# Performance work log

Hardware: AMD Instinct MI355X
Metric: run time of the kernel (lower is better)

The kernel has to match this reference:

```python
import jax, jax.numpy as jnp
import numpy as np

NQ = 8          # qubits -> 2^8 = 256 amplitudes
B = 32768       # batch

# ---- gate matrices (torchquantum conventions) ----

def _rx(t):
    c = jnp.cos(t / 2).astype(jnp.complex64)
    s = jnp.sin(t / 2).astype(jnp.complex64)
    return jnp.stack([jnp.stack([c, -1j * s]), jnp.stack([-1j * s, c])])

def _ry(t):
    c = jnp.cos(t / 2).astype(jnp.complex64)
    s = jnp.sin(t / 2).astype(jnp.complex64)
    return jnp.stack([jnp.stack([c, -s]), jnp.stack([s, c])])

def _rz(t):
    tc = t.astype(jnp.complex64)
    z = jnp.zeros((), jnp.complex64)
    return jnp.stack([jnp.stack([jnp.exp(-0.5j * tc), z]),
                      jnp.stack([z, jnp.exp(0.5j * tc)])])

def _u3(p):
    th, ph, lm = p[0], p[1], p[2]
    ct = jnp.cos(th / 2).astype(jnp.complex64)
    st = jnp.sin(th / 2).astype(jnp.complex64)
    eip = jnp.exp(1j * ph.astype(jnp.complex64))
    eil = jnp.exp(1j * lm.astype(jnp.complex64))
    return jnp.stack([jnp.stack([ct, -eil * st]),
                      jnp.stack([eip * st, eip * eil * ct])])

# ---- statevector ops; state shape [B] + [2]*NQ ----

def apply_1q(state, U, w):
    s = jnp.moveaxis(state, 1 + w, -1)
    s = jnp.einsum('ij,b...j->b...i', U, s)
    return jnp.moveaxis(s, -1, 1 + w)

def apply_ctrl(state, U, c, t):
    s = jnp.moveaxis(state, (1 + c, 1 + t), (-2, -1))
    s1 = jnp.einsum('ij,b...j->b...i', U, s[..., 1, :])
    s = jnp.concatenate([s[..., :1, :], s1[..., None, :]], axis=-2)
    return jnp.moveaxis(s, (-2, -1), (1 + c, 1 + t))

def expval_z(state, w):
    p = state.real ** 2 + state.imag ** 2
    axes = tuple(i for i in range(1, NQ + 1) if i != 1 + w)
    pm = jnp.sum(p, axis=axes)  # [B, 2]
    return pm[:, 0] - pm[:, 1]

def encode(x):
    # RY angle encoding: product state, amplitude per qubit = (cos(x/2), sin(x/2))
    a = jnp.stack([jnp.cos(x / 2), jnp.sin(x / 2)], -1).astype(jnp.complex64)  # [B,8,2]
    state = a[:, 0]
    for q in range(1, NQ):
        state = jnp.einsum('b...i,bj->b...ij', state, a[:, q])
    return state  # [B,2,2,...,2]

CR_PAIRS_1 = [(0, 1), (2, 3), (4, 5), (6, 7), (1, 2), (3, 4), (5, 6)]
CR_PAIRS_2 = [(1, 3), (5, 7), (3, 5)]

def branch(state, cr_fn, crp, u3p):
    # crp: [10] angles, u3p: [6,3]
    for i, (c, t) in enumerate(CR_PAIRS_1):
        state = apply_ctrl(state, cr_fn(crp[i]), c, t)
    # intermediate tqm.expval calls do not mutate the state -> omitted
    for i, w in enumerate([1, 3, 5, 7]):
        state = apply_1q(state, _u3(u3p[i]), w)
    for i, (c, t) in enumerate(CR_PAIRS_2):
        state = apply_ctrl(state, cr_fn(crp[7 + i]), c, t)
    state = apply_1q(state, _u3(u3p[4]), 3)
    state = apply_1q(state, _u3(u3p[5]), 7)
    return jnp.stack([expval_z(state, 3), expval_z(state, 7)], axis=1)  # [B,2]


def setup_inputs() -> dict:
    key = jax.random.key(0)
    ks = jax.random.split(key, 12)
    pi = np.float32(np.pi)
    u = lambda k, shape: jax.random.uniform(k, shape, jnp.float32, -pi, pi)
    return {
        'x': u(ks[0], (B, NQ)),
        'crx_params': u(ks[1], (10,)),
        'u3x_params': u(ks[2], (6, 3)),
        'cry_params': u(ks[3], (10,)),
        'u3y_params': u(ks[4], (6, 3)),
        'crz_params': u(ks[5], (10,)),
        'u3z_params': u(ks[6], (6, 3)),
        'w1': jax.random.normal(ks[7], (12, 6), jnp.float32) * 0.3,
        'b1': jnp.zeros((12,), jnp.float32),
        'w2': jax.random.normal(ks[8], (1, 12), jnp.float32) * 0.3,
        'b2': jnp.zeros((1,), jnp.float32),
    }


def reference(x, crx_params, u3x_params, cry_params, u3y_params,
              crz_params, u3z_params, w1, b1, w2, b2):
    state = encode(x)
    fx = branch(state, _rx, crx_params, u3x_params)  # CRX branch (qdev)
    fy = branch(state, _ry, cry_params, u3y_params)  # CRY branch (qdev1)
    fz = branch(state, _rz, crz_params, u3z_params)  # CRZ branch (qdev2)
    feats = jnp.concatenate([fx, fy, fz], axis=1)    # [B,6]
    h = jnp.tanh(feats @ w1.T + b1)
    return jax.nn.sigmoid(h @ w2.T + b2)             # [B,1]
```

## Files before the change

kernel.cpp:

```cpp
#include <hip/hip_runtime.h>
#include <math.h>


typedef float v2f __attribute__((ext_vector_type(2)));

__device__ __forceinline__ v2f mk2(float a, float b) { v2f r; r.x = a; r.y = b; return r; }

__device__ __forceinline__ v2f pk_mul_s(v2f a, v2f b) {
  v2f d;
  asm("v_pk_mul_f32 %0, %1, %2 op_sel:[0,0] op_sel_hi:[0,1]"
      : "=v"(d) : "v"(a), "v"(b));
  return d;
}
__device__ __forceinline__ v2f pk_fma_slo(v2f a, v2f b, v2f c) {
  v2f d;
  asm("v_pk_fma_f32 %0, %1, %2, %3 op_sel:[0,0,0] op_sel_hi:[0,1,1]"
      : "=v"(d) : "v"(a), "v"(b), "v"(c));
  return d;
}
__device__ __forceinline__ v2f pk_fma_shi(v2f a, v2f b, v2f c) {
  v2f d;
  asm("v_pk_fma_f32 %0, %1, %2, %3 op_sel:[1,0,0] op_sel_hi:[1,1,1]"
      : "=v"(d) : "v"(a), "v"(b), "v"(c));
  return d;
}
__device__ __forceinline__ v2f pk_fma_shi_neg(v2f a, v2f b, v2f c) {
  v2f d;
  asm("v_pk_fma_f32 %0, %1, %2, %3 op_sel:[1,0,0] op_sel_hi:[1,1,1] neg_lo:[1,0,0] neg_hi:[1,0,0]"
      : "=v"(d) : "v"(a), "v"(b), "v"(c));
  return d;
}
__device__ __forceinline__ v2f pk_fma_rot(v2f a, v2f b, v2f c) {
  v2f d;
  asm("v_pk_fma_f32 %0, %1, %2, %3 op_sel:[1,1,0] op_sel_hi:[1,0,1] neg_hi:[0,1,0]"
      : "=v"(d) : "v"(a), "v"(b), "v"(c));
  return d;
}
__device__ __forceinline__ v2f pk_fma_irot(v2f a, v2f b, v2f c) {
  v2f d;
  asm("v_pk_fma_f32 %0, %1, %2, %3 op_sel:[1,1,0] op_sel_hi:[1,0,1] neg_lo:[0,1,0]"
      : "=v"(d) : "v"(a), "v"(b), "v"(c));
  return d;
}
__device__ __forceinline__ v2f cmul(v2f a, v2f b) {
  return pk_fma_irot(a, b, pk_mul_s(a, b));
}

template <int MASK>
__device__ __forceinline__ float swz1(float v) {
  constexpr int pat = (MASK << 10) | 0x1F;
  return __int_as_float(__builtin_amdgcn_ds_swizzle(__float_as_int(v), pat));
}
template <int MASK>
__device__ __forceinline__ v2f swz2(v2f v) {
  v2f r;
  r.x = swz1<MASK>(v.x);
  r.y = swz1<MASK>(v.y);
  return r;
}

__device__ __forceinline__ v2f ld2(const float* __restrict__ p) {
  return *(const v2f*)p;
}

template <bool A_REAL>
__device__ __forceinline__ v2f u3row(v2f ua, v2f ub, v2f a, v2f b) {
  v2f t = pk_mul_s(ua, a);
  if constexpr (!A_REAL) t = pk_fma_irot(ua, a, t);
  t = pk_fma_slo(ub, b, t);
  return pk_fma_irot(ub, b, t);
}

template <int KIND, int SB, int LB>
__device__ __forceinline__ void cr_Sc_Lt(v2f w[16], v2f cs, int gl) {
  v2f K = cs;
  if constexpr (KIND == 1) {
    const bool tb = (gl >> LB) & 1;
    K.y = tb ? K.y : -K.y;
  }
  if constexpr (KIND == 2) {
    const bool tb = (gl >> LB) & 1;
    K.y = tb ? -K.y : K.y;
  }
#pragma unroll
  for (int s = 0; s < 16; ++s) {
    if (!(s & (1 << SB))) continue;
    if constexpr (KIND == 2) {
      const v2f t = pk_mul_s(K, w[s]);
      w[s] = pk_fma_rot(K, w[s], t);
    } else {
      const v2f p = swz2<(1 << LB)>(w[s]);
      const v2f t = pk_mul_s(K, w[s]);
      if constexpr (KIND == 0)
        w[s] = pk_fma_rot(K, p, t);
      else
        w[s] = pk_fma_shi(K, p, t);
    }
  }
}

template <int KIND, int SBc, int SBt>
__device__ __forceinline__ void cr_Sc_St(v2f w[16], v2f cs) {
#pragma unroll
  for (int s0 = 0; s0 < 16; ++s0) {
    if (!(s0 & (1 << SBc))) continue;
    if (s0 & (1 << SBt)) continue;
    const int s1 = s0 | (1 << SBt);
    if constexpr (KIND == 2) {
      const v2f t0 = pk_mul_s(cs, w[s0]);
      w[s0] = pk_fma_rot(cs, w[s0], t0);
      const v2f t1 = pk_mul_s(cs, w[s1]);
      w[s1] = pk_fma_irot(cs, w[s1], t1);
    } else {
      const v2f a = w[s0], b = w[s1];
      if constexpr (KIND == 0) {
        w[s0] = pk_fma_rot(cs, b, pk_mul_s(cs, a));
        w[s1] = pk_fma_rot(cs, a, pk_mul_s(cs, b));
      } else {
        w[s0] = pk_fma_shi_neg(cs, b, pk_mul_s(cs, a));
        w[s1] = pk_fma_shi(cs, a, pk_mul_s(cs, b));
      }
    }
  }
}

template <int SB>
__device__ __forceinline__ void u3_apply(v2f w[16], const float* __restrict__ p) {
  const v2f M0 = ld2(p), M1 = ld2(p + 2), M2 = ld2(p + 4), M3 = ld2(p + 6);
#pragma unroll
  for (int s0 = 0; s0 < 16; ++s0) {
    if (s0 & (1 << SB)) continue;
    const int s1 = s0 | (1 << SB);
    const v2f a = w[s0], b = w[s1];
    w[s0] = u3row<true>(M0, M1, a, b);
    w[s1] = u3row<false>(M3, M2, b, a);
  }
}

template <int SB, int CB, bool M00R>
__device__ __forceinline__ void u3_sel(v2f w[16], const float* __restrict__ pM,
                                       const float* __restrict__ pN) {
  const v2f M0 = ld2(pM), M1 = ld2(pM + 2), M2 = ld2(pM + 4), M3 = ld2(pM + 6);
  const v2f N0 = ld2(pN), N1 = ld2(pN + 2), N2 = ld2(pN + 4), N3 = ld2(pN + 6);
#pragma unroll
  for (int s0 = 0; s0 < 16; ++s0) {
    if (s0 & (1 << SB)) continue;
    const int s1 = s0 | (1 << SB);
    const v2f a = w[s0], b = w[s1];
    if ((s0 >> CB) & 1) {
      w[s0] = u3row<false>(N0, N1, a, b);
      w[s1] = u3row<false>(N3, N2, b, a);
    } else {
      w[s0] = u3row<M00R>(M0, M1, a, b);
      w[s1] = u3row<false>(M3, M2, b, a);
    }
  }
}

template <int KIND>
__device__ __forceinline__ void pairvals(float c, float s, const float* pp,
                                         v2f out[4]) {
  out[0] = mk2(pp[0], 0.f);
  out[1] = mk2(pp[1], 0.f);
  const float u = pp[2], wv = pp[3];
  if constexpr (KIND == 0) {
    out[2] = mk2(c * u, -s * wv);
    out[3] = mk2(c * wv, -s * u);
  } else if constexpr (KIND == 1) {
    out[2] = mk2(c * u - s * wv, 0.f);
    out[3] = mk2(s * u + c * wv, 0.f);
  } else {
    out[2] = mk2(c * u, -s * u);
    out[3] = mk2(c * wv, s * wv);
  }
}

template <int KIND>
__device__ __forceinline__ v2f run_branch(const float pp[4][4],
                                          const float* __restrict__ Gb,
                                          int gl) {
  v2f P01[4], P23[4], P45[4], P67[4];
  pairvals<KIND>(Gb[0], Gb[1], pp[0], P01);
  pairvals<KIND>(Gb[8], Gb[9], pp[1], P23);
  pairvals<KIND>(Gb[16], Gb[17], pp[2], P45);
  pairvals<KIND>(Gb[24], Gb[25], pp[3], P67);
  const bool l0 = gl & 1, l1 = (gl >> 1) & 1, l2 = (gl >> 2) & 1,
             l3 = (gl >> 3) & 1;
  v2f s01[2] = {l0 ? P01[2] : P01[0], l0 ? P01[3] : P01[1]};
  v2f s23[2] = {l1 ? P23[2] : P23[0], l1 ? P23[3] : P23[1]};
  v2f s45[2] = {l2 ? P45[2] : P45[0], l2 ? P45[3] : P45[1]};
  v2f s67[2] = {l3 ? P67[2] : P67[0], l3 ? P67[3] : P67[1]};
  v2f A[4], Bv[4];
  A[0] = cmul(s01[0], s45[0]);
  A[1] = cmul(s01[0], s45[1]);
  A[2] = cmul(s01[1], s45[0]);
  A[3] = cmul(s01[1], s45[1]);
  Bv[0] = cmul(s67[0], s23[0]);
  Bv[1] = cmul(s67[0], s23[1]);
  Bv[2] = cmul(s67[1], s23[0]);
  Bv[3] = cmul(s67[1], s23[1]);
  v2f w[16];
#pragma unroll
  for (int s = 0; s < 16; ++s) w[s] = cmul(A[s >> 2], Bv[s & 3]);

  cr_Sc_Lt<KIND, 3, 1>(w, ld2(Gb + 32), gl);
  cr_Sc_Lt<KIND, 0, 2>(w, ld2(Gb + 40), gl);
  cr_Sc_Lt<KIND, 2, 3>(w, ld2(Gb + 48), gl);
  u3_apply<3>(w, Gb + 64);
  u3_sel<0, 3, true>(w, Gb + 72, Gb + 80);
  u3_apply<2>(w, Gb + 88);
  u3_sel<1, 2, false>(w, Gb + 96, Gb + 104);
  cr_Sc_St<KIND, 0, 2>(w, ld2(Gb + 56));
  u3_apply<0>(w, Gb + 112);

  float p[16];
#pragma unroll
  for (int s = 0; s < 16; ++s)
    p[s] = __builtin_fmaf(w[s].x, w[s].x, w[s].y * w[s].y);
  float g[4];
#pragma unroll
  for (int j = 0; j < 4; ++j)
    g[j] = (p[j] + p[j + 4]) + (p[j + 8] + p[j + 12]);
  float z3 = (g[0] + g[2]) - (g[1] + g[3]);
  float z7 = (g[0] + g[1]) - (g[2] + g[3]);
  z3 += swz1<1>(z3); z7 += swz1<1>(z7);
  z3 += swz1<2>(z3); z7 += swz1<2>(z7);
  z3 += swz1<4>(z3); z7 += swz1<4>(z7);
  z3 += swz1<8>(z3); z7 += swz1<8>(z7);
  return mk2(z3, z7);
}

struct c2 { float r, i; };
__device__ __forceinline__ c2 cmulh(c2 a, c2 b) {
  return {a.r * b.r - a.i * b.i, a.r * b.i + a.i * b.r};
}
__device__ __forceinline__ c2 caddh(c2 a, c2 b) { return {a.r + b.r, a.i + b.i}; }
__device__ void mat2mul(const c2 A[4], const c2 B[4], c2 C[4]) {
  C[0] = caddh(cmulh(A[0], B[0]), cmulh(A[1], B[2]));
  C[1] = caddh(cmulh(A[0], B[1]), cmulh(A[1], B[3]));
  C[2] = caddh(cmulh(A[2], B[0]), cmulh(A[3], B[2]));
  C[3] = caddh(cmulh(A[2], B[1]), cmulh(A[3], B[3]));
}
__device__ void u3m(const float* p, c2 M[4]) {
  float st, ct, sp, cp, sl, cl;
  sincosf(0.5f * p[0], &st, &ct);
  sincosf(p[1], &sp, &cp);
  sincosf(p[2], &sl, &cl);
  M[0] = {ct, 0.f};
  M[1] = {-cl * st, -sl * st};
  M[2] = {cp * st, sp * st};
  M[3] = {(cp * cl - sp * sl) * ct, (sp * cl + cp * sl) * ct};
}
__device__ void rmat(int kind, float th, c2 R[4]) {
  float s, c;
  sincosf(0.5f * th, &s, &c);
  if (kind == 0) {
    R[0] = {c, 0.f}; R[1] = {0.f, -s}; R[2] = {0.f, -s}; R[3] = {c, 0.f};
  } else if (kind == 1) {
    R[0] = {c, 0.f}; R[1] = {-s, 0.f}; R[2] = {s, 0.f}; R[3] = {c, 0.f};
  } else {
    R[0] = {c, -s}; R[1] = {0.f, 0.f}; R[2] = {0.f, 0.f}; R[3] = {c, s};
  }
}
__device__ void storeM(float* dst, const c2 M[4]) {
#pragma unroll
  for (int j = 0; j < 4; ++j) { dst[2 * j] = M[j].r; dst[2 * j + 1] = M[j].i; }
}

__global__ void qcnn_prep(const float* __restrict__ crx, const float* __restrict__ u3x,
                          const float* __restrict__ cry, const float* __restrict__ u3y,
                          const float* __restrict__ crz, const float* __restrict__ u3z,
                          float* __restrict__ G) {
  const int br = threadIdx.x;
  if (br >= 3) return;
  const float* crp = (br == 0) ? crx : (br == 1) ? cry : crz;
  const float* u3p = (br == 0) ? u3x : (br == 1) ? u3y : u3z;
  float* Gb = G + br * 128;

  const int crIdx[8] = {0, 1, 2, 3, 4, 5, 6, 9};
#pragma unroll
  for (int i = 0; i < 8; ++i) {
    float s, c;
    sincosf(0.5f * crp[crIdx[i]], &s, &c);
    Gb[i * 8] = c;
    Gb[i * 8 + 1] = s;
  }
  c2 U1v[4], U3v[4], U5v[4], U7a[4], U7b[4], U3f[4], R[4], T[4], T2[4];
  u3m(u3p + 0, U1v);
  u3m(u3p + 3, U3v);
  u3m(u3p + 6, U5v);
  u3m(u3p + 9, U7a);
  u3m(u3p + 12, U3f);
  u3m(u3p + 15, U7b);
  storeM(Gb + 64, U1v);
  storeM(Gb + 72, U3v);
  rmat(br, crp[7], R);
  mat2mul(R, U3v, T);
  storeM(Gb + 80, T);
  storeM(Gb + 88, U5v);
  mat2mul(U7b, U7a, T);
  storeM(Gb + 96, T);
  rmat(br, crp[8], R);
  mat2mul(R, U7a, T);
  mat2mul(U7b, T, T2);
  storeM(Gb + 104, T2);
  storeM(Gb + 112, U3f);
}

__global__ __launch_bounds__(256) void qcnn_main(
    const float* __restrict__ x, const float* __restrict__ G,
    const float* __restrict__ w1, const float* __restrict__ b1,
    const float* __restrict__ w2, const float* __restrict__ b2,
    float* __restrict__ out, int B) {
  const int gid = blockIdx.x * blockDim.x + threadIdx.x;
  const int b = gid >> 4;
  const int gl = threadIdx.x & 15;
  if (b >= B) return;

  const float4* xv = reinterpret_cast<const float4*>(x + b * 8);
  const float4 xlo = xv[0], xhi = xv[1];
  const float xq[8] = {xlo.x, xlo.y, xlo.z, xlo.w, xhi.x, xhi.y, xhi.z, xhi.w};
  float sn[8], cs_[8];
#pragma unroll
  for (int q = 0; q < 8; ++q) __sincosf(0.5f * xq[q], &sn[q], &cs_[q]);
  float pp[4][4];
#pragma unroll
  for (int pr = 0; pr < 4; ++pr) {
    const int qc = 2 * pr, qt = 2 * pr + 1;
    pp[pr][0] = cs_[qc] * cs_[qt];
    pp[pr][1] = cs_[qc] * sn[qt];
    pp[pr][2] = sn[qc] * cs_[qt];
    pp[pr][3] = sn[qc] * sn[qt];
  }

  const v2f fx = run_branch<0>(pp, G, gl);
  const v2f fy = run_branch<1>(pp, G + 128, gl);
  const v2f fz = run_branch<2>(pp, G + 256, gl);

  const int j = (gl < 12) ? gl : 0;
  const float* w1r = w1 + j * 6;
  float a = b1[j];
  a += w1r[0] * fx.x + w1r[1] * fx.y + w1r[2] * fy.x + w1r[3] * fy.y +
       w1r[4] * fz.x + w1r[5] * fz.y;
  const float e = __expf(2.f * a);
  const float th = 1.f - 2.f * __builtin_amdgcn_rcpf(e + 1.f);
  float t = (gl < 12) ? w2[j] * th : 0.f;
  t += swz1<1>(t);
  t += swz1<2>(t);
  t += swz1<4>(t);
  t += swz1<8>(t);
  const float acc = t + b2[0];
  const float res = __builtin_amdgcn_rcpf(1.f + __expf(-acc));
  if (gl == 0) out[b] = res;
}

extern "C" void kernel_launch(void* const* d_in, const int* in_sizes, int n_in,
                              void* d_out, int out_size, void* d_ws,
                              size_t ws_size, hipStream_t stream) {
  const float* x = (const float*)d_in[0];
  const float* crx = (const float*)d_in[1];
  const float* u3x = (const float*)d_in[2];
  const float* cry = (const float*)d_in[3];
  const float* u3y = (const float*)d_in[4];
  const float* crz = (const float*)d_in[5];
  const float* u3z = (const float*)d_in[6];
  const float* w1 = (const float*)d_in[7];
  const float* b1 = (const float*)d_in[8];
  const float* w2 = (const float*)d_in[9];
  const float* b2 = (const float*)d_in[10];
  float* out = (float*)d_out;
  float* G = (float*)d_ws;
  const int B = in_sizes[0] / 8;

  hipLaunchKernelGGL(qcnn_prep, dim3(1), dim3(64), 0, stream, crx, u3x, cry,
                     u3y, crz, u3z, G);
  const int threads = 256;
  const int blocks = (B * 16 + threads - 1) / threads;
  hipLaunchKernelGGL(qcnn_main, dim3(blocks), dim3(threads), 0, stream, x, G,
                     w1, b1, w2, b2, out, B);
}
```

Measured before the change: 108.7 us.

## Specialize each rotation branch algebraically and fold final U3 into measurement

Splits the generic branch into per-gate specializations. The RY branch runs its early gates in real arithmetic, and the RZ branch computes its early controlled-RZ gates as closed-form phases followed by per-amplitude sincos. The final U3 is folded into precomputed measurement coefficients, and gate matrices are passed as SGPR operands in the packed-math asm. It also recomputes sincos of the inputs per branch and sets occupancy launch bounds. This aims to cut VALU work, with the cost of more code complexity and redundant sincos per branch.

```diff
diff --git a/kernel.cpp b/kernel.cpp
--- a/kernel.cpp
+++ b/kernel.cpp
@@ -5,46 +5,28 @@
 typedef float v2f __attribute__((ext_vector_type(2)));
 
 __device__ __forceinline__ v2f mk2(float a, float b) { v2f r; r.x = a; r.y = b; return r; }
-
-__device__ __forceinline__ v2f pk_mul_s(v2f a, v2f b) {
-  v2f d;
-  asm("v_pk_mul_f32 %0, %1, %2 op_sel:[0,0] op_sel_hi:[0,1]"
-      : "=v"(d) : "v"(a), "v"(b));
-  return d;
-}
-__device__ __forceinline__ v2f pk_fma_slo(v2f a, v2f b, v2f c) {
-  v2f d;
-  asm("v_pk_fma_f32 %0, %1, %2, %3 op_sel:[0,0,0] op_sel_hi:[0,1,1]"
-      : "=v"(d) : "v"(a), "v"(b), "v"(c));
-  return d;
-}
-__device__ __forceinline__ v2f pk_fma_shi(v2f a, v2f b, v2f c) {
-  v2f d;
-  asm("v_pk_fma_f32 %0, %1, %2, %3 op_sel:[1,0,0] op_sel_hi:[1,1,1]"
-      : "=v"(d) : "v"(a), "v"(b), "v"(c));
-  return d;
-}
-__device__ __forceinline__ v2f pk_fma_shi_neg(v2f a, v2f b, v2f c) {
-  v2f d;
-  asm("v_pk_fma_f32 %0, %1, %2, %3 op_sel:[1,0,0] op_sel_hi:[1,1,1] neg_lo:[1,0,0] neg_hi:[1,0,0]"
-      : "=v"(d) : "v"(a), "v"(b), "v"(c));
-  return d;
-}
-__device__ __forceinline__ v2f pk_fma_rot(v2f a, v2f b, v2f c) {
-  v2f d;
-  asm("v_pk_fma_f32 %0, %1, %2, %3 op_sel:[1,1,0] op_sel_hi:[1,0,1] neg_hi:[0,1,0]"
-      : "=v"(d) : "v"(a), "v"(b), "v"(c));
-  return d;
-}
-__device__ __forceinline__ v2f pk_fma_irot(v2f a, v2f b, v2f c) {
-  v2f d;
-  asm("v_pk_fma_f32 %0, %1, %2, %3 op_sel:[1,1,0] op_sel_hi:[1,0,1] neg_lo:[0,1,0]"
-      : "=v"(d) : "v"(a), "v"(b), "v"(c));
-  return d;
-}
-__device__ __forceinline__ v2f cmul(v2f a, v2f b) {
-  return pk_fma_irot(a, b, pk_mul_s(a, b));
-}
+__device__ __forceinline__ v2f ld2(const float* __restrict__ p) { return *(const v2f*)p; }
+
+__device__ __forceinline__ v2f pk_mul_s(v2f a, v2f b) { v2f d;
+  asm("v_pk_mul_f32 %0, %1, %2 op_sel:[0,0] op_sel_hi:[0,1]" : "=v"(d) : "v"(a), "v"(b)); return d; }
+__device__ __forceinline__ v2f pk_fma_irot(v2f a, v2f b, v2f c) { v2f d;
+  asm("v_pk_fma_f32 %0, %1, %2, %3 op_sel:[1,1,0] op_sel_hi:[1,0,1] neg_lo:[0,1,0]" : "=v"(d) : "v"(a), "v"(b), "v"(c)); return d; }
+__device__ __forceinline__ v2f cmul(v2f a, v2f b) { return pk_fma_irot(a, b, pk_mul_s(a, b)); }
+__device__ __forceinline__ v2f pk_mul_swap(v2f a, v2f b) { v2f d;
+  asm("v_pk_mul_f32 %0, %1, %2 op_sel:[1,0] op_sel_hi:[0,1]" : "=v"(d) : "v"(a), "v"(b)); return d; }
+
+__device__ __forceinline__ v2f pk_mul_sM(v2f M, v2f b) { v2f d;
+  asm("v_pk_mul_f32 %0, %1, %2 op_sel:[0,0] op_sel_hi:[0,1]" : "=v"(d) : "s"(M), "v"(b)); return d; }
+__device__ __forceinline__ v2f pk_fma_sloM(v2f M, v2f b, v2f c) { v2f d;
+  asm("v_pk_fma_f32 %0, %1, %2, %3 op_sel:[0,0,0] op_sel_hi:[0,1,1]" : "=v"(d) : "s"(M), "v"(b), "v"(c)); return d; }
+__device__ __forceinline__ v2f pk_fma_shiM(v2f M, v2f b, v2f c) { v2f d;
+  asm("v_pk_fma_f32 %0, %1, %2, %3 op_sel:[1,0,0] op_sel_hi:[1,1,1]" : "=v"(d) : "s"(M), "v"(b), "v"(c)); return d; }
+__device__ __forceinline__ v2f pk_fma_shi_negM(v2f M, v2f b, v2f c) { v2f d;
+  asm("v_pk_fma_f32 %0, %1, %2, %3 op_sel:[1,0,0] op_sel_hi:[1,1,1] neg_lo:[1,0,0] neg_hi:[1,0,0]" : "=v"(d) : "s"(M), "v"(b), "v"(c)); return d; }
+__device__ __forceinline__ v2f pk_fma_rotM(v2f M, v2f b, v2f c) { v2f d;
+  asm("v_pk_fma_f32 %0, %1, %2, %3 op_sel:[1,1,0] op_sel_hi:[1,0,1] neg_hi:[0,1,0]" : "=v"(d) : "s"(M), "v"(b), "v"(c)); return d; }
+__device__ __forceinline__ v2f pk_fma_irotM(v2f M, v2f b, v2f c) { v2f d;
+  asm("v_pk_fma_f32 %0, %1, %2, %3 op_sel:[1,1,0] op_sel_hi:[1,0,1] neg_lo:[0,1,0]" : "=v"(d) : "s"(M), "v"(b), "v"(c)); return d; }
 
 template <int MASK>
 __device__ __forceinline__ float swz1(float v) {
@@ -53,75 +35,15 @@
 }
 template <int MASK>
 __device__ __forceinline__ v2f swz2(v2f v) {
-  v2f r;
-  r.x = swz1<MASK>(v.x);
-  r.y = swz1<MASK>(v.y);
-  return r;
-}
-
-__device__ __forceinline__ v2f ld2(const float* __restrict__ p) {
-  return *(const v2f*)p;
+  v2f r; r.x = swz1<MASK>(v.x); r.y = swz1<MASK>(v.y); return r;
 }
 
 template <bool A_REAL>
-__device__ __forceinline__ v2f u3row(v2f ua, v2f ub, v2f a, v2f b) {
-  v2f t = pk_mul_s(ua, a);
-  if constexpr (!A_REAL) t = pk_fma_irot(ua, a, t);
-  t = pk_fma_slo(ub, b, t);
-  return pk_fma_irot(ub, b, t);
-}
-
-template <int KIND, int SB, int LB>
-__device__ __forceinline__ void cr_Sc_Lt(v2f w[16], v2f cs, int gl) {
-  v2f K = cs;
-  if constexpr (KIND == 1) {
-    const bool tb = (gl >> LB) & 1;
-    K.y = tb ? K.y : -K.y;
-  }
-  if constexpr (KIND == 2) {
-    const bool tb = (gl >> LB) & 1;
-    K.y = tb ? -K.y : K.y;
-  }
-#pragma unroll
-  for (int s = 0; s < 16; ++s) {
-    if (!(s & (1 << SB))) continue;
-    if constexpr (KIND == 2) {
-      const v2f t = pk_mul_s(K, w[s]);
-      w[s] = pk_fma_rot(K, w[s], t);
-    } else {
-      const v2f p = swz2<(1 << LB)>(w[s]);
-      const v2f t = pk_mul_s(K, w[s]);
-      if constexpr (KIND == 0)
-        w[s] = pk_fma_rot(K, p, t);
-      else
-        w[s] = pk_fma_shi(K, p, t);
-    }
-  }
-}
-
-template <int KIND, int SBc, int SBt>
-__device__ __forceinline__ void cr_Sc_St(v2f w[16], v2f cs) {
-#pragma unroll
-  for (int s0 = 0; s0 < 16; ++s0) {
-    if (!(s0 & (1 << SBc))) continue;
-    if (s0 & (1 << SBt)) continue;
-    const int s1 = s0 | (1 << SBt);
-    if constexpr (KIND == 2) {
-      const v2f t0 = pk_mul_s(cs, w[s0]);
-      w[s0] = pk_fma_rot(cs, w[s0], t0);
-      const v2f t1 = pk_mul_s(cs, w[s1]);
-      w[s1] = pk_fma_irot(cs, w[s1], t1);
-    } else {
-      const v2f a = w[s0], b = w[s1];
-      if constexpr (KIND == 0) {
-        w[s0] = pk_fma_rot(cs, b, pk_mul_s(cs, a));
-        w[s1] = pk_fma_rot(cs, a, pk_mul_s(cs, b));
-      } else {
-        w[s0] = pk_fma_shi_neg(cs, b, pk_mul_s(cs, a));
-        w[s1] = pk_fma_shi(cs, a, pk_mul_s(cs, b));
-      }
-    }
-  }
+__device__ __forceinline__ v2f u3row_s(v2f ua, v2f ub, v2f a, v2f b) {
+  v2f t = pk_mul_sM(ua, a);
+  if constexpr (!A_REAL) t = pk_fma_irotM(ua, a, t);
+  t = pk_fma_sloM(ub, b, t);
+  return pk_fma_irotM(ub, b, t);
 }
 
 template <int SB>
@@ -132,8 +54,8 @@
     if (s0 & (1 << SB)) continue;
     const int s1 = s0 | (1 << SB);
     const v2f a = w[s0], b = w[s1];
-    w[s0] = u3row<true>(M0, M1, a, b);
-    w[s1] = u3row<false>(M3, M2, b, a);
+    w[s0] = u3row_s<true>(M0, M1, a, b);
+    w[s1] = u3row_s<false>(M3, M2, b, a);
   }
 }
 
@@ -148,81 +70,96 @@
     const int s1 = s0 | (1 << SB);
     const v2f a = w[s0], b = w[s1];
     if ((s0 >> CB) & 1) {
-      w[s0] = u3row<false>(N0, N1, a, b);
-      w[s1] = u3row<false>(N3, N2, b, a);
+      w[s0] = u3row_s<false>(N0, N1, a, b);
+      w[s1] = u3row_s<false>(N3, N2, b, a);
     } else {
-      w[s0] = u3row<M00R>(M0, M1, a, b);
-      w[s1] = u3row<false>(M3, M2, b, a);
+      w[s0] = u3row_s<M00R>(M0, M1, a, b);
+      w[s1] = u3row_s<false>(M3, M2, b, a);
     }
   }
 }
 
-template <int KIND>
-__device__ __forceinline__ void pairvals(float c, float s, const float* pp,
-                                         v2f out[4]) {
-  out[0] = mk2(pp[0], 0.f);
-  out[1] = mk2(pp[1], 0.f);
-  const float u = pp[2], wv = pp[3];
-  if constexpr (KIND == 0) {
-    out[2] = mk2(c * u, -s * wv);
-    out[3] = mk2(c * wv, -s * u);
-  } else if constexpr (KIND == 1) {
-    out[2] = mk2(c * u - s * wv, 0.f);
-    out[3] = mk2(s * u + c * wv, 0.f);
-  } else {
-    out[2] = mk2(c * u, -s * u);
-    out[3] = mk2(c * wv, s * wv);
-  }
-}
-
-template <int KIND>
-__device__ __forceinline__ v2f run_branch(const float pp[4][4],
-                                          const float* __restrict__ Gb,
-                                          int gl) {
-  v2f P01[4], P23[4], P45[4], P67[4];
-  pairvals<KIND>(Gb[0], Gb[1], pp[0], P01);
-  pairvals<KIND>(Gb[8], Gb[9], pp[1], P23);
-  pairvals<KIND>(Gb[16], Gb[17], pp[2], P45);
-  pairvals<KIND>(Gb[24], Gb[25], pp[3], P67);
-  const bool l0 = gl & 1, l1 = (gl >> 1) & 1, l2 = (gl >> 2) & 1,
-             l3 = (gl >> 3) & 1;
-  v2f s01[2] = {l0 ? P01[2] : P01[0], l0 ? P01[3] : P01[1]};
-  v2f s23[2] = {l1 ? P23[2] : P23[0], l1 ? P23[3] : P23[1]};
-  v2f s45[2] = {l2 ? P45[2] : P45[0], l2 ? P45[3] : P45[1]};
-  v2f s67[2] = {l3 ? P67[2] : P67[0], l3 ? P67[3] : P67[1]};
-  v2f A[4], Bv[4];
-  A[0] = cmul(s01[0], s45[0]);
-  A[1] = cmul(s01[0], s45[1]);
-  A[2] = cmul(s01[1], s45[0]);
-  A[3] = cmul(s01[1], s45[1]);
-  Bv[0] = cmul(s67[0], s23[0]);
-  Bv[1] = cmul(s67[0], s23[1]);
-  Bv[2] = cmul(s67[1], s23[0]);
-  Bv[3] = cmul(s67[1], s23[1]);
-  v2f w[16];
-#pragma unroll
-  for (int s = 0; s < 16; ++s) w[s] = cmul(A[s >> 2], Bv[s & 3]);
-
-  cr_Sc_Lt<KIND, 3, 1>(w, ld2(Gb + 32), gl);
-  cr_Sc_Lt<KIND, 0, 2>(w, ld2(Gb + 40), gl);
-  cr_Sc_Lt<KIND, 2, 3>(w, ld2(Gb + 48), gl);
-  u3_apply<3>(w, Gb + 64);
-  u3_sel<0, 3, true>(w, Gb + 72, Gb + 80);
-  u3_apply<2>(w, Gb + 88);
-  u3_sel<1, 2, false>(w, Gb + 96, Gb + 104);
-  cr_Sc_St<KIND, 0, 2>(w, ld2(Gb + 56));
-  u3_apply<0>(w, Gb + 112);
-
-  float p[16];
-#pragma unroll
-  for (int s = 0; s < 16; ++s)
-    p[s] = __builtin_fmaf(w[s].x, w[s].x, w[s].y * w[s].y);
-  float g[4];
-#pragma unroll
-  for (int j = 0; j < 4; ++j)
-    g[j] = (p[j] + p[j + 4]) + (p[j + 8] + p[j + 12]);
-  float z3 = (g[0] + g[2]) - (g[1] + g[3]);
-  float z7 = (g[0] + g[1]) - (g[2] + g[3]);
+template <int SB, int LB>
+__device__ __forceinline__ void crx_Sc_Lt(v2f w[16], v2f cs) {
+#pragma unroll
+  for (int s = 0; s < 16; ++s) {
+    if (!(s & (1 << SB))) continue;
+    const v2f p = swz2<(1 << LB)>(w[s]);
+    w[s] = pk_fma_rotM(cs, p, pk_mul_sM(cs, w[s]));
+  }
+}
+
+template <int SB, int LB>
+__device__ __forceinline__ void cr_ry_r(float w[16], v2f cs, int gl) {
+  const bool tb = (gl >> LB) & 1;
+  const float Ky = tb ? cs.y : -cs.y;
+#pragma unroll
+  for (int s = 0; s < 16; ++s) {
+    if (!(s & (1 << SB))) continue;
+    const float p = swz1<(1 << LB)>(w[s]);
+    w[s] = __builtin_fmaf(Ky, p, cs.x * w[s]);
+  }
+}
+
+template <int KIND, int SBc, int SBt>
+__device__ __forceinline__ void cr_Sc_St(v2f w[16], v2f cs) {
+#pragma unroll
+  for (int s0 = 0; s0 < 16; ++s0) {
+    if (!(s0 & (1 << SBc))) continue;
+    if constexpr (KIND == 2) {
+      const v2f t = pk_mul_sM(cs, w[s0]);
+      w[s0] = (s0 & (1 << SBt)) ? pk_fma_irotM(cs, w[s0], t)
+                                : pk_fma_rotM(cs, w[s0], t);
+    } else {
+      if (s0 & (1 << SBt)) continue;
+      const int s1 = s0 | (1 << SBt);
+      const v2f a = w[s0], b = w[s1];
+      if constexpr (KIND == 0) {
+        w[s0] = pk_fma_rotM(cs, b, pk_mul_sM(cs, a));
+        w[s1] = pk_fma_rotM(cs, a, pk_mul_sM(cs, b));
+      } else {
+        w[s0] = pk_fma_shi_negM(cs, b, pk_mul_sM(cs, a));
+        w[s1] = pk_fma_shiM(cs, a, pk_mul_sM(cs, b));
+      }
+    }
+  }
+}
+
+template <int SB>
+__device__ __forceinline__ void u3_lift(v2f w[16], const float wr[16],
+                                        const float* __restrict__ p) {
+  const v2f M0 = ld2(p), M1 = ld2(p + 2), M2 = ld2(p + 4), M3 = ld2(p + 6);
+#pragma unroll
+  for (int s0 = 0; s0 < 16; ++s0) {
+    if (s0 & (1 << SB)) continue;
+    const int s1 = s0 | (1 << SB);
+    const float a = wr[s0], b = wr[s1];
+    w[s0] = mk2(__builtin_fmaf(a, M0.x, b * M1.x), b * M1.y);
+    w[s1] = mk2(__builtin_fmaf(a, M2.x, b * M3.x),
+                __builtin_fmaf(a, M2.y, b * M3.y));
+  }
+}
+
+__device__ __forceinline__ v2f measure(v2f w[16], const float* __restrict__ q) {
+  const v2f qa = ld2(q);
+  const v2f qg = ld2(q + 2);
+  float z3a = 0.f, z3b = 0.f, z7p = 0.f, z7m = 0.f;
+#pragma unroll
+  for (int s0 = 0; s0 < 16; s0 += 2) {
+    const v2f a = w[s0], b = w[s0 + 1];
+    const v2f t1 = a * b, t2 = pk_mul_swap(a, b), t3 = a * a, t4 = b * b;
+    const float r = t1.x + t1.y;
+    const float m = t2.x - t2.y;
+    const float na = t3.x + t3.y;
+    const float nb = t4.x + t4.y;
+    z3a = __builtin_fmaf(qa.x, na, z3a);
+    z3b = __builtin_fmaf(qa.y, nb, z3b);
+    z3a = __builtin_fmaf(qg.x, r, z3a);
+    z3b = __builtin_fmaf(-qg.y, m, z3b);
+    const float nn = na + nb;
+    if (s0 & 2) z7m += nn; else z7p += nn;
+  }
+  float z3 = z3a + z3b, z7 = z7p - z7m;
   z3 += swz1<1>(z3); z7 += swz1<1>(z7);
   z3 += swz1<2>(z3); z7 += swz1<2>(z7);
   z3 += swz1<4>(z3); z7 += swz1<4>(z7);
@@ -230,10 +167,130 @@
   return mk2(z3, z7);
 }
 
+template <int KIND>
+__device__ __forceinline__ v2f tail_common(v2f w[16], const float* __restrict__ Gb) {
+  u3_sel<0, 3, true>(w, Gb + 72, Gb + 80);
+  u3_apply<2>(w, Gb + 88);
+  u3_sel<1, 2, false>(w, Gb + 96, Gb + 104);
+  cr_Sc_St<KIND, 0, 2>(w, ld2(Gb + 56));
+  return measure(w, Gb + 112);
+}
+
+__device__ __forceinline__ void load_sincos(const float* __restrict__ xb,
+                                            float sn[8], float cn[8]) {
+  const float4 xlo = ((const float4*)xb)[0];
+  const float4 xhi = ((const float4*)xb)[1];
+  const float xq[8] = {xlo.x, xlo.y, xlo.z, xlo.w, xhi.x, xhi.y, xhi.z, xhi.w};
+#pragma unroll
+  for (int q = 0; q < 8; ++q) __sincosf(0.5f * xq[q], &sn[q], &cn[q]);
+}
+
+__device__ v2f run_rx(const float* __restrict__ xb, const float* __restrict__ Gb,
+                      int gl) {
+  float sn[8], cn[8];
+  load_sincos(xb, sn, cn);
+  const bool l0 = gl & 1, l1 = (gl >> 1) & 1, l2 = (gl >> 2) & 1, l3 = (gl >> 3) & 1;
+  v2f pa[4], pb[4];
+#pragma unroll
+  for (int pr = 0; pr < 4; ++pr) {
+    const bool lh = (pr == 0) ? l0 : (pr == 1) ? l1 : (pr == 2) ? l2 : l3;
+    const float c = Gb[pr * 8], s = Gb[pr * 8 + 1];
+    const float uc = lh ? sn[2 * pr] : cn[2 * pr];
+    const float b0 = uc * cn[2 * pr + 1], b1 = uc * sn[2 * pr + 1];
+    const float Kx = lh ? c : 1.f;
+    const float Kyn = lh ? -s : 0.f;
+    pa[pr] = mk2(Kx * b0, Kyn * b1);
+    pb[pr] = mk2(Kx * b1, Kyn * b0);
+  }
+  v2f A[4] = {cmul(pa[0], pa[2]), cmul(pa[0], pb[2]), cmul(pb[0], pa[2]), cmul(pb[0], pb[2])};
+  v2f Bv[4] = {cmul(pa[3], pa[1]), cmul(pa[3], pb[1]), cmul(pb[3], pa[1]), cmul(pb[3], pb[1])};
+  v2f w[16];
+#pragma unroll
+  for (int s = 0; s < 16; ++s) w[s] = cmul(A[s >> 2], Bv[s & 3]);
+  crx_Sc_Lt<3, 1>(w, ld2(Gb + 32));
+  crx_Sc_Lt<0, 2>(w, ld2(Gb + 40));
+  crx_Sc_Lt<2, 3>(w, ld2(Gb + 48));
+  u3_apply<3>(w, Gb + 64);
+  return tail_common<0>(w, Gb);
+}
+
+__device__ v2f run_ry(const float* __restrict__ xb, const float* __restrict__ Gb,
+                      int gl) {
+  float sn[8], cn[8];
+  load_sincos(xb, sn, cn);
+  const bool l0 = gl & 1, l1 = (gl >> 1) & 1, l2 = (gl >> 2) & 1, l3 = (gl >> 3) & 1;
+  float pa[4], pb[4];
+#pragma unroll
+  for (int pr = 0; pr < 4; ++pr) {
+    const bool lh = (pr == 0) ? l0 : (pr == 1) ? l1 : (pr == 2) ? l2 : l3;
+    const float c = Gb[pr * 8], s = Gb[pr * 8 + 1];
+    const float uc = lh ? sn[2 * pr] : cn[2 * pr];
+    const float b0 = uc * cn[2 * pr + 1], b1 = uc * sn[2 * pr + 1];
+    const float Kx = lh ? c : 1.f;
+    const float Ky = lh ? s : 0.f;
+    pa[pr] = Kx * b0 - Ky * b1;
+    pb[pr] = Ky * b0 + Kx * b1;
+  }
+  const float A[4] = {pa[0] * pa[2], pa[0] * pb[2], pb[0] * pa[2], pb[0] * pb[2]};
+  const float Bv[4] = {pa[3] * pa[1], pa[3] * pb[1], pb[3] * pa[1], pb[3] * pb[1]};
+  float wr[16];
+#pragma unroll
+  for (int s = 0; s < 16; ++s) wr[s] = A[s >> 2] * Bv[s & 3];
+  cr_ry_r<3, 1>(wr, ld2(Gb + 32), gl);
+  cr_ry_r<0, 2>(wr, ld2(Gb + 40), gl);
+  cr_ry_r<2, 3>(wr, ld2(Gb + 48), gl);
+  v2f w[16];
+  u3_lift<3>(w, wr, Gb + 64);
+  return tail_common<1>(w, Gb);
+}
+
+__device__ v2f run_rz(const float* __restrict__ xb, const float* __restrict__ Gb,
+                      int gl) {
+  float sn[8], cn[8];
+  load_sincos(xb, sn, cn);
+  const bool l0 = gl & 1, l1 = (gl >> 1) & 1, l2 = (gl >> 2) & 1, l3 = (gl >> 3) & 1;
+  const float u0 = l0 ? sn[0] : cn[0];
+  const float u2 = l1 ? sn[2] : cn[2];
+  const float u4 = l2 ? sn[4] : cn[4];
+  const float u6 = l3 ? sn[6] : cn[6];
+  const float P = (u0 * u2) * (u4 * u6);
+  float v01[4], v23[4];
+  v01[0] = P * (cn[3] * cn[7]); v01[1] = P * (sn[3] * cn[7]);
+  v01[2] = P * (cn[3] * sn[7]); v01[3] = P * (sn[3] * sn[7]);
+  v23[0] = cn[5] * cn[1]; v23[1] = sn[5] * cn[1];
+  v23[2] = cn[5] * sn[1]; v23[3] = sn[5] * sn[1];
+  const float t0 = Gb[2], h0 = Gb[3];
+  const float t1 = Gb[10], h1 = Gb[11];
+  const float t2 = Gb[18], h2 = Gb[19];
+  const float t3 = Gb[26], h3 = Gb[27];
+  const float h4 = Gb[35], h5 = Gb[43], h6 = Gb[51];
+  const float kk[4] = {(l1 ? t1 : 0.f) + (l2 ? h5 : -h5),
+                       (l3 ? t3 : 0.f),
+                       (l2 ? t2 : 0.f) + (l3 ? h6 : -h6),
+                       (l0 ? t0 : 0.f) + (l1 ? h4 : -h4)};
+  const float aa = -((l0 ? h0 : 0.f) + (l1 ? h1 : 0.f) + (l2 ? h2 : 0.f) + (l3 ? h3 : 0.f));
+  float ph[16];
+  ph[0] = aa;
+#pragma unroll
+  for (int bb = 0; bb < 4; ++bb) {
+#pragma unroll
+    for (int s = 0; s < (1 << bb); ++s) ph[s | (1 << bb)] = ph[s] + kk[bb];
+  }
+  v2f w[16];
+#pragma unroll
+  for (int s = 0; s < 16; ++s) {
+    float sp, cp;
+    __sincosf(ph[s], &sp, &cp);
+    const float e = v01[s & 3] * v23[s >> 2];
+    w[s] = mk2(e * cp, e * sp);
+  }
+  u3_apply<3>(w, Gb + 64);
+  return tail_common<2>(w, Gb);
+}
+
 struct c2 { float r, i; };
-__device__ __forceinline__ c2 cmulh(c2 a, c2 b) {
-  return {a.r * b.r - a.i * b.i, a.r * b.i + a.i * b.r};
-}
+__device__ __forceinline__ c2 cmulh(c2 a, c2 b) { return {a.r * b.r - a.i * b.i, a.r * b.i + a.i * b.r}; }
+__device__ __forceinline__ c2 cmulc(c2 a, c2 b) { return {a.r * b.r + a.i * b.i, a.i * b.r - a.r * b.i}; }
 __device__ __forceinline__ c2 caddh(c2 a, c2 b) { return {a.r + b.r, a.i + b.i}; }
 __device__ void mat2mul(const c2 A[4], const c2 B[4], c2 C[4]) {
   C[0] = caddh(cmulh(A[0], B[0]), cmulh(A[1], B[2]));
@@ -254,13 +311,9 @@
 __device__ void rmat(int kind, float th, c2 R[4]) {
   float s, c;
   sincosf(0.5f * th, &s, &c);
-  if (kind == 0) {
-    R[0] = {c, 0.f}; R[1] = {0.f, -s}; R[2] = {0.f, -s}; R[3] = {c, 0.f};
-  } else if (kind == 1) {
-    R[0] = {c, 0.f}; R[1] = {-s, 0.f}; R[2] = {s, 0.f}; R[3] = {c, 0.f};
-  } else {
-    R[0] = {c, -s}; R[1] = {0.f, 0.f}; R[2] = {0.f, 0.f}; R[3] = {c, s};
-  }
+  if (kind == 0) { R[0] = {c, 0.f}; R[1] = {0.f, -s}; R[2] = {0.f, -s}; R[3] = {c, 0.f}; }
+  else if (kind == 1) { R[0] = {c, 0.f}; R[1] = {-s, 0.f}; R[2] = {s, 0.f}; R[3] = {c, 0.f}; }
+  else { R[0] = {c, -s}; R[1] = {0.f, 0.f}; R[2] = {0.f, 0.f}; R[3] = {c, s}; }
 }
 __device__ void storeM(float* dst, const c2 M[4]) {
 #pragma unroll
@@ -280,10 +333,13 @@
   const int crIdx[8] = {0, 1, 2, 3, 4, 5, 6, 9};
 #pragma unroll
   for (int i = 0; i < 8; ++i) {
+    const float th = crp[crIdx[i]];
     float s, c;
-    sincosf(0.5f * crp[crIdx[i]], &s, &c);
+    sincosf(0.5f * th, &s, &c);
     Gb[i * 8] = c;
     Gb[i * 8 + 1] = s;
+    Gb[i * 8 + 2] = th;
+    Gb[i * 8 + 3] = 0.5f * th;
   }
   c2 U1v[4], U3v[4], U5v[4], U7a[4], U7b[4], U3f[4], R[4], T[4], T2[4];
   u3m(u3p + 0, U1v);
@@ -304,10 +360,19 @@
   mat2mul(R, U7a, T);
   mat2mul(U7b, T, T2);
   storeM(Gb + 104, T2);
-  storeM(Gb + 112, U3f);
-}
-
-__global__ __launch_bounds__(256) void qcnn_main(
+  const float n00 = U3f[0].r * U3f[0].r + U3f[0].i * U3f[0].i;
+  const float n01 = U3f[1].r * U3f[1].r + U3f[1].i * U3f[1].i;
+  const float n10 = U3f[2].r * U3f[2].r + U3f[2].i * U3f[2].i;
+  const float n11 = U3f[3].r * U3f[3].r + U3f[3].i * U3f[3].i;
+  const c2 g01 = cmulc(U3f[0], U3f[1]);
+  const c2 g23 = cmulc(U3f[2], U3f[3]);
+  Gb[112] = n00 - n10;
+  Gb[113] = n01 - n11;
+  Gb[114] = 2.f * (g01.r - g23.r);
+  Gb[115] = 2.f * (g01.i - g23.i);
+}
+
+__global__ __launch_bounds__(256, 8) void qcnn_main(
     const float* __restrict__ x, const float* __restrict__ G,
     const float* __restrict__ w1, const float* __restrict__ b1,
     const float* __restrict__ w2, const float* __restrict__ b2,
@@ -316,26 +381,11 @@
   const int b = gid >> 4;
   const int gl = threadIdx.x & 15;
   if (b >= B) return;
-
-  const float4* xv = reinterpret_cast<const float4*>(x + b * 8);
-  const float4 xlo = xv[0], xhi = xv[1];
-  const float xq[8] = {xlo.x, xlo.y, xlo.z, xlo.w, xhi.x, xhi.y, xhi.z, xhi.w};
-  float sn[8], cs_[8];
-#pragma unroll
-  for (int q = 0; q < 8; ++q) __sincosf(0.5f * xq[q], &sn[q], &cs_[q]);
-  float pp[4][4];
-#pragma unroll
-  for (int pr = 0; pr < 4; ++pr) {
-    const int qc = 2 * pr, qt = 2 * pr + 1;
-    pp[pr][0] = cs_[qc] * cs_[qt];
-    pp[pr][1] = cs_[qc] * sn[qt];
-    pp[pr][2] = sn[qc] * cs_[qt];
-    pp[pr][3] = sn[qc] * sn[qt];
-  }
-
-  const v2f fx = run_branch<0>(pp, G, gl);
-  const v2f fy = run_branch<1>(pp, G + 128, gl);
-  const v2f fz = run_branch<2>(pp, G + 256, gl);
+  const float* xb = x + b * 8;
+
+  const v2f fx = run_rx(xb, G, gl);
+  const v2f fy = run_ry(xb, G + 128, gl);
+  const v2f fz = run_rz(xb, G + 256, gl);
 
   const int j = (gl < 12) ? gl : 0;
   const float* w1r = w1 + j * 6;
```

After: 107.8 us. About the same (-0.8%).
